# Optimization experiments

Measured on AMD Instinct MI355X. Metric: run time of the kernel, lower is better.

## Reference

```python
import jax, jax.numpy as jnp
import numpy as np

EMBED_DIM = 1024
NUM_HEADS = 16
DIM_K = EMBED_DIM // NUM_HEADS
B, S = 2, 2048


def setup_inputs() -> dict:
    key = jax.random.key(0)
    ks = jax.random.split(key, 7)
    scale = 1.0 / np.sqrt(EMBED_DIM)
    return {
        "query": jax.random.normal(ks[0], (B, S, EMBED_DIM), dtype=jnp.float32),
        "key": jax.random.normal(ks[1], (B, S, EMBED_DIM), dtype=jnp.float32),
        "value": jax.random.normal(ks[2], (B, S, EMBED_DIM), dtype=jnp.float32),
        "Wq": jax.random.normal(ks[3], (EMBED_DIM, EMBED_DIM), dtype=jnp.float32) * scale,
        "Wk": jax.random.normal(ks[4], (EMBED_DIM, EMBED_DIM), dtype=jnp.float32) * scale,
        "Wv": jax.random.normal(ks[5], (EMBED_DIM, EMBED_DIM), dtype=jnp.float32) * scale,
        "Wo": jax.random.normal(ks[6], (EMBED_DIM, EMBED_DIM), dtype=jnp.float32) * scale,
    }


def reference(query, key, value, Wq, Wk, Wv, Wo):
    b, s, e = query.shape
    # nn.Linear: y = x @ W.T  (bias=False)
    def proj(x, W):
        y = x @ W.T  # [b, s, e]
        return y.reshape(b, -1, NUM_HEADS, DIM_K).transpose(0, 2, 1, 3)  # [b, h, s, dk]

    q = proj(query, Wq)
    k = proj(key, Wk)
    v = proj(value, Wv)

    # attention: scores = q k^T / sqrt(dk); softmax; @ v  (dropout p=0 in eval)
    scores = jnp.einsum("bhqd,bhkd->bhqk", q, k) / jnp.sqrt(jnp.float32(DIM_K))
    attn = jax.nn.softmax(scores, axis=-1)
    x = jnp.einsum("bhqk,bhkd->bhqd", attn, v)  # [b, h, s, dk]

    x = x.transpose(0, 2, 1, 3).reshape(b, -1, e)  # merge heads
    return x @ Wo.T
```

## Files before the change

### kernel.cpp

```cpp
#include <hip/hip_runtime.h>
#include <hip/hip_bf16.h>
#include <stdint.h>

#define EMBED 1024
#define NHEAD 16
#define DKD   64
#define BATCH 2
#define SEQ   2048
#define MROWS (BATCH*SEQ)

typedef __attribute__((ext_vector_type(8)))  short bf16x8;
typedef __attribute__((ext_vector_type(4)))  float f32x4;
typedef __attribute__((ext_vector_type(16))) float f32x16;
typedef unsigned short u16;
typedef unsigned int   u32;
typedef __attribute__((ext_vector_type(4))) u32 u32x4;

__device__ inline u16 f2bf(float f) {
  return __builtin_bit_cast(u16, __float2bfloat16(f));
}

__device__ inline u32 cvtpk(float lo, float hi) {
  u32 r;
  asm("v_cvt_pk_bf16_f32 %0, %1, %2" : "=v"(r) : "v"(lo), "v"(hi));
  return r;
}

__device__ inline void plswap(u32& x, u32& y) {
  asm volatile("v_permlane32_swap_b32 %0, %1" : "+v"(x), "+v"(y));
}

__device__ inline void gload_lds16(const u16* g, u16* l) {
  __builtin_amdgcn_global_load_lds(
      (const __attribute__((address_space(1))) u32*)(const void*)g,
      (__attribute__((address_space(3))) u32*)(void*)l, 16, 0, 0);
}

__global__ __launch_bounds__(256) void cast_w(
    const float* __restrict__ s0, const float* __restrict__ s1,
    const float* __restrict__ s2, const float* __restrict__ s3,
    u16* __restrict__ d0, u16* __restrict__ d1, u16* __restrict__ d2,
    u16* __restrict__ d3) {
  const int y = blockIdx.y;
  const float* s = (y == 0) ? s0 : (y == 1) ? s1 : (y == 2) ? s2 : s3;
  u16* d        = (y == 0) ? d0 : (y == 1) ? d1 : (y == 2) ? d2 : d3;
  constexpr int n4 = EMBED * EMBED / 4;
  int i = blockIdx.x * 256 + threadIdx.x;
  int stride = gridDim.x * 256;
  for (int idx = i; idx < n4; idx += stride) {
    float4 f = ((const float4*)s)[idx];
    ushort4 o;
    o.x = f2bf(f.x); o.y = f2bf(f.y); o.z = f2bf(f.z); o.w = f2bf(f.w);
    ((ushort4*)d)[idx] = o;
  }
}

__global__ __launch_bounds__(256)
void gemm_qkv(const float* __restrict__ A0, const float* __restrict__ A1,
              const float* __restrict__ A2, const u16* __restrict__ B0,
              const u16* __restrict__ B1, const u16* __restrict__ B2,
              u16* __restrict__ C0, u16* __restrict__ C1, u16* __restrict__ C2) {
  constexpr int K = EMBED;
  __shared__ u16 As[128 * 32];
  __shared__ u16 Bs[128 * 32];
  const int z = blockIdx.z;
  const float* A = (z == 0) ? A0 : (z == 1) ? A1 : A2;
  const u16* B   = (z == 0) ? B0 : (z == 1) ? B1 : B2;
  u16* C         = (z == 0) ? C0 : (z == 1) ? C1 : C2;

  const int t = threadIdx.x;
  const int w = t >> 6, l = t & 63;
  const int lr = l & 15, lg = l >> 4;
  const int fid = blockIdx.x;
  const int mblk = 4 * (fid & 7) + (fid >> 6);
  const int nblk = (fid >> 3) & 7;
  const int m0 = mblk * 128;
  const int n0 = nblk * 128;
  const int wr = (w >> 1) * 64, wc = (w & 1) * 64;

  f32x4 acc[4][4] = {};

  const int srow = t >> 2;
  const int scol = (t & 3) * 8;
  const float* Agf = A + (size_t)(m0 + srow) * K + scol;
  const u16*   Bg  = B + (size_t)(n0 + srow) * K + scol;
  u16* BsW = Bs + w * 512;
  const size_t rowstep = (size_t)64 * K;

  auto loadA = [&](float4 (&f)[4], int k0) {
    f[0] = *(const float4*)(Agf + k0);
    f[1] = *(const float4*)(Agf + k0 + 4);
    f[2] = *(const float4*)(Agf + k0 + rowstep);
    f[3] = *(const float4*)(Agf + k0 + rowstep + 4);
  };

  float4 fa[4];
  loadA(fa, 0);
  for (int k0 = 0; k0 < K; k0 += 32) {
    u32x4 pa0 = {cvtpk(fa[0].x, fa[0].y), cvtpk(fa[0].z, fa[0].w),
                 cvtpk(fa[1].x, fa[1].y), cvtpk(fa[1].z, fa[1].w)};
    u32x4 pa1 = {cvtpk(fa[2].x, fa[2].y), cvtpk(fa[2].z, fa[2].w),
                 cvtpk(fa[3].x, fa[3].y), cvtpk(fa[3].z, fa[3].w)};
    *(u32x4*)(As + w * 512 + l * 8)        = pa0;
    *(u32x4*)(As + 2048 + w * 512 + l * 8) = pa1;
    gload_lds16(Bg + k0,           BsW);
    gload_lds16(Bg + k0 + rowstep, BsW + 64 * 32);
    if (k0 + 32 < K) loadA(fa, k0 + 32);
    __syncthreads();
    bf16x8 a[4], b[4];
#pragma unroll
    for (int r = 0; r < 4; r++)
      a[r] = *(const bf16x8*)(As + (wr + r * 16 + lr) * 32 + 8 * lg);
#pragma unroll
    for (int c = 0; c < 4; c++)
      b[c] = *(const bf16x8*)(Bs + (wc + c * 16 + lr) * 32 + 8 * lg);
#pragma unroll
    for (int r = 0; r < 4; r++)
#pragma unroll
      for (int c = 0; c < 4; c++)
        acc[r][c] = __builtin_amdgcn_mfma_f32_16x16x32_bf16(a[r], b[c], acc[r][c], 0, 0, 0);
    __syncthreads();
  }

  const float esc = (z == 0) ? 0.18033688f : 1.0f;
#pragma unroll
  for (int r = 0; r < 4; r++)
#pragma unroll
    for (int c = 0; c < 4; c++)
#pragma unroll
      for (int j = 0; j < 4; j++) {
        int m = m0 + wr + r * 16 + lg * 4 + j;
        int n = n0 + wc + c * 16 + lr;
        int b_ = m >> 11, s_ = m & 2047;
        int h_ = n >> 6,  d_ = n & 63;
        u16 vv = f2bf(acc[r][c][j] * esc);
        if (z == 2)
          C[((size_t)(b_ * NHEAD + h_) * DKD + d_) * SEQ + s_] = vv;
        else
          C[(((size_t)(b_ * NHEAD + h_) * SEQ + s_) << 6) + d_] = vv;
      }
}

__global__ __launch_bounds__(256)
void gemm_out(const u16* __restrict__ A, const u16* __restrict__ B,
              float* __restrict__ C) {
  constexpr int K = EMBED, N = EMBED;
  __shared__ u16 As[64 * 32];
  __shared__ u16 Bs[128 * 32];
  const int t = threadIdx.x;
  const int w = t >> 6, l = t & 63;
  const int lr = l & 15, lg = l >> 4;
  const int fid = blockIdx.x;
  const int mblk = 8 * (fid & 7) + (fid >> 6);
  const int nblk = (fid >> 3) & 7;
  const int m0 = mblk * 64;
  const int n0 = nblk * 128;
  const int wr = (w >> 1) * 32, wc = (w & 1) * 64;

  f32x4 acc[2][4] = {};

  const int srow = t >> 2;
  const int scol = (t & 3) * 8;
  const u16* Ag = A + (size_t)(m0 + srow) * K + scol;
  const u16* Bg = B + (size_t)(n0 + srow) * K + scol;
  u16* AsW = As + w * 512;
  u16* BsW = Bs + w * 512;
  const size_t rowstep = (size_t)64 * K;

  for (int k0 = 0; k0 < K; k0 += 32) {
    gload_lds16(Ag + k0,           AsW);
    gload_lds16(Bg + k0,           BsW);
    gload_lds16(Bg + k0 + rowstep, BsW + 64 * 32);
    __syncthreads();
    bf16x8 a[2], b[4];
#pragma unroll
    for (int r = 0; r < 2; r++)
      a[r] = *(const bf16x8*)(As + (wr + r * 16 + lr) * 32 + 8 * lg);
#pragma unroll
    for (int c = 0; c < 4; c++)
      b[c] = *(const bf16x8*)(Bs + (wc + c * 16 + lr) * 32 + 8 * lg);
#pragma unroll
    for (int r = 0; r < 2; r++)
#pragma unroll
      for (int c = 0; c < 4; c++)
        acc[r][c] = __builtin_amdgcn_mfma_f32_16x16x32_bf16(a[r], b[c], acc[r][c], 0, 0, 0);
    __syncthreads();
  }

#pragma unroll
  for (int r = 0; r < 2; r++)
#pragma unroll
    for (int c = 0; c < 4; c++)
#pragma unroll
      for (int j = 0; j < 4; j++) {
        int m = m0 + wr + r * 16 + lg * 4 + j;
        int n = n0 + wc + c * 16 + lr;
        C[(size_t)m * N + n] = acc[r][c][j];
      }
}

__global__ __launch_bounds__(256, 2)
void attn_kernel(const u16* __restrict__ Qh, const u16* __restrict__ Kh,
                 const u16* __restrict__ Vt, u16* __restrict__ Xo) {
  __shared__ u16 KV[4][8192];
  const int t = threadIdx.x, w = t >> 6, l = t & 63;
  const int q32 = l & 31, h = l >> 5;
  const int xcd = blockIdx.x & 7;
  const int li  = blockIdx.x >> 3;
  const int bh  = xcd * 4 + (li >> 4);
  const int qblk = li & 15;
  const int b_ = bh >> 4, h_ = bh & 15;
  const size_t base = (size_t)bh * SEQ * DKD;
  const u16* Kb = Kh + base;
  const u16* Vb = Vt + base;
  constexpr int NT = SEQ / 64;
  constexpr float NM = -1.442695041f;

  const int qrow = qblk * 128 + w * 32 + q32;
  bf16x8 qf[4];
#pragma unroll
  for (int ks = 0; ks < 4; ks++)
    qf[ks] = *(const bf16x8*)(Qh + base + (size_t)qrow * DKD + ks * 16 + h * 8);

  const u32 one2 = 0x3F803F80u;
  const bf16x8 ones = __builtin_bit_cast(bf16x8, (u32x4){one2, one2, one2, one2});
  f32x16 nmv;
#pragma unroll
  for (int r = 0; r < 16; r++) nmv[r] = NM;

  f32x16 acc[2] = {};
  f32x16 lacc = {};

  auto stage = [&](int slot, int kt) {
    u16* kd = &KV[slot][0];
    u16* vd = &KV[slot][4096];
    const int rb = w * 8 + (l >> 3);
    const int sg = (l & 7) ^ (l >> 3);
#pragma unroll
    for (int ch = 0; ch < 2; ch++) {
      int row = ch * 32 + rb;
      gload_lds16(Kb + (size_t)(kt * 64 + row) * DKD + sg * 8,
                  kd + (ch * 32 + w * 8) * 64);
      gload_lds16(Vb + (size_t)row * SEQ + kt * 64 + sg * 8,
                  vd + (ch * 32 + w * 8) * 64);
    }
  };

  auto qk = [&](const u16* kd, f32x16 (&s)[2]) {
#pragma unroll
    for (int c = 0; c < 2; c++) {
      int row = c * 32 + q32;
#pragma unroll
      for (int ks = 0; ks < 4; ks++) {
        bf16x8 kf = *(const bf16x8*)(kd + row * 64 + (((2 * ks + h) ^ (row & 7)) * 8));
        s[c] = __builtin_amdgcn_mfma_f32_32x32x16_bf16(kf, qf[ks], s[c], 0, 0, 0);
      }
    }
  };
  auto vload = [&](const u16* vd, bf16x8 (&vf)[2][4]) {
#pragma unroll
    for (int dc = 0; dc < 2; dc++) {
      int row = dc * 32 + q32;
#pragma unroll
      for (int tile = 0; tile < 4; tile++)
        vf[dc][tile] = *(const bf16x8*)(vd + row * 64 + (((2 * tile + h) ^ (row & 7)) * 8));
    }
  };
  auto exp_pack = [&](f32x16 (&s)[2], bf16x8 (&pfrag)[4]) {
#pragma unroll
    for (int c = 0; c < 2; c++) {
      float p[16];
#pragma unroll
      for (int r = 0; r < 16; r++)
        p[r] = __builtin_amdgcn_exp2f(s[c][r]);
      u32 Pk[8];
#pragma unroll
      for (int i = 0; i < 8; i++) Pk[i] = cvtpk(p[2 * i], p[2 * i + 1]);
      plswap(Pk[0], Pk[2]); plswap(Pk[1], Pk[3]);
      plswap(Pk[4], Pk[6]); plswap(Pk[5], Pk[7]);
      pfrag[2 * c]     = __builtin_bit_cast(bf16x8, (u32x4){Pk[0], Pk[1], Pk[2], Pk[3]});
      pfrag[2 * c + 1] = __builtin_bit_cast(bf16x8, (u32x4){Pk[4], Pk[5], Pk[6], Pk[7]});
    }
  };
  auto pv = [&](bf16x8 (&vf)[2][4], bf16x8 (&pfrag)[4]) {
#pragma unroll
    for (int tile = 0; tile < 4; tile++) {
#pragma unroll
      for (int dc = 0; dc < 2; dc++)
        acc[dc] = __builtin_amdgcn_mfma_f32_32x32x16_bf16(vf[dc][tile], pfrag[tile], acc[dc], 0, 0, 0);
      lacc = __builtin_amdgcn_mfma_f32_32x32x16_bf16(ones, pfrag[tile], lacc, 0, 0, 0);
    }
  };

  stage(0, 0);
  stage(1, 1);
  __syncthreads();

  for (int kt = 0; kt < NT; kt += 2) {
    const int sA = kt & 3, sB = (kt + 1) & 3;
    if (kt + 2 < NT) {
      stage((kt + 2) & 3, kt + 2);
      stage((kt + 3) & 3, kt + 3);
    }
    f32x16 scA[2], scB[2];
    scA[0] = nmv; scA[1] = nmv; scB[0] = nmv; scB[1] = nmv;
    qk(&KV[sA][0], scA);
    qk(&KV[sB][0], scB);
    bf16x8 vfA[2][4];
    vload(&KV[sA][4096], vfA);
    bf16x8 pfA[4];
    exp_pack(scA, pfA);
    pv(vfA, pfA);
    bf16x8 vfB[2][4];
    vload(&KV[sB][4096], vfB);
    bf16x8 pfB[4];
    exp_pack(scB, pfB);
    pv(vfB, pfB);
    __syncthreads();
  }

  float inv = 1.0f / lacc[0];
  u16* orow = Xo + ((size_t)b_ * SEQ + qrow) * EMBED + h_ * DKD;
#pragma unroll
  for (int dc = 0; dc < 2; dc++)
#pragma unroll
    for (int k4 = 0; k4 < 4; k4++) {
      u32 w0 = cvtpk(acc[dc][4 * k4 + 0] * inv, acc[dc][4 * k4 + 1] * inv);
      u32 w1 = cvtpk(acc[dc][4 * k4 + 2] * inv, acc[dc][4 * k4 + 3] * inv);
      int d = dc * 32 + k4 * 8 + h * 4;
      uint2 pk; pk.x = w0; pk.y = w1;
      *(uint2*)(orow + d) = pk;
    }
}

extern "C" void kernel_launch(void* const* d_in, const int* in_sizes, int n_in,
                              void* d_out, int out_size, void* d_ws, size_t ws_size,
                              hipStream_t stream) {
  const float* q  = (const float*)d_in[0];
  const float* k  = (const float*)d_in[1];
  const float* v  = (const float*)d_in[2];
  const float* Wq = (const float*)d_in[3];
  const float* Wk = (const float*)d_in[4];
  const float* Wv = (const float*)d_in[5];
  const float* Wo = (const float*)d_in[6];

  char* ws = (char*)d_ws;
  const size_t SZ_X = (size_t)MROWS * EMBED * 2;
  const size_t SZ_W = (size_t)EMBED * EMBED * 2;
  u16* wqb  = (u16*)(ws + 3 * SZ_X);
  u16* wkb  = (u16*)(ws + 3 * SZ_X + SZ_W);
  u16* wvb  = (u16*)(ws + 3 * SZ_X + 2 * SZ_W);
  u16* wob  = (u16*)(ws + 3 * SZ_X + 3 * SZ_W);
  u16* Qh   = (u16*)(ws + 3 * SZ_X + 4 * SZ_W);
  u16* Kh   = (u16*)(ws + 4 * SZ_X + 4 * SZ_W);
  u16* Vt   = (u16*)(ws + 5 * SZ_X + 4 * SZ_W);
  u16* Xcat = (u16*)(ws + 6 * SZ_X + 4 * SZ_W);

  cast_w<<<dim3(128, 4), 256, 0, stream>>>(Wq, Wk, Wv, Wo, wqb, wkb, wvb, wob);

  gemm_qkv<<<dim3(256, 1, 3), 256, 0, stream>>>(
      q, k, v, wqb, wkb, wvb, Qh, Kh, Vt);

  attn_kernel<<<512, 256, 0, stream>>>(Qh, Kh, Vt, Xcat);

  gemm_out<<<512, 256, 0, stream>>>(Xcat, wob, (float*)d_out);
}
```

Before: 110.6 us.

## Stage fp32 A tiles directly to LDS via async loads, convert on read

The QKV projection GEMM now copies fp32 activation tiles straight into shared memory with global_load_lds, using an XOR-swizzled layout. Conversion to bf16 happens after the LDS read instead of before the LDS write. This drops the register prefetch and conversion stage. In exchange it doubles the LDS footprint for A, converts each value redundantly across waves, and loses the overlap the previous register prefetch gave between the next tile's global load and the current tile's compute.

```diff
diff --git a/kernel.cpp b/kernel.cpp
--- a/kernel.cpp
+++ b/kernel.cpp
@@ -31,6 +31,11 @@
 }
 
 __device__ inline void gload_lds16(const u16* g, u16* l) {
+  __builtin_amdgcn_global_load_lds(
+      (const __attribute__((address_space(1))) u32*)(const void*)g,
+      (__attribute__((address_space(3))) u32*)(void*)l, 16, 0, 0);
+}
+__device__ inline void gload_lds16f(const float* g, float* l) {
   __builtin_amdgcn_global_load_lds(
       (const __attribute__((address_space(1))) u32*)(const void*)g,
       (__attribute__((address_space(3))) u32*)(void*)l, 16, 0, 0);
@@ -61,8 +66,8 @@
               const u16* __restrict__ B1, const u16* __restrict__ B2,
               u16* __restrict__ C0, u16* __restrict__ C1, u16* __restrict__ C2) {
   constexpr int K = EMBED;
-  __shared__ u16 As[128 * 32];
-  __shared__ u16 Bs[128 * 32];
+  __shared__ float Asf[128 * 32];
+  __shared__ u16   Bs[128 * 32];
   const int z = blockIdx.z;
   const float* A = (z == 0) ? A0 : (z == 1) ? A1 : A2;
   const u16* B   = (z == 0) ? B0 : (z == 1) ? B1 : B2;
@@ -82,35 +87,36 @@
 
   const int srow = t >> 2;
   const int scol = (t & 3) * 8;
-  const float* Agf = A + (size_t)(m0 + srow) * K + scol;
-  const u16*   Bg  = B + (size_t)(n0 + srow) * K + scol;
+  const u16* Bg = B + (size_t)(n0 + srow) * K + scol;
   u16* BsW = Bs + w * 512;
   const size_t rowstep = (size_t)64 * K;
 
-  auto loadA = [&](float4 (&f)[4], int k0) {
-    f[0] = *(const float4*)(Agf + k0);
-    f[1] = *(const float4*)(Agf + k0 + 4);
-    f[2] = *(const float4*)(Agf + k0 + rowstep);
-    f[3] = *(const float4*)(Agf + k0 + rowstep + 4);
-  };
-
-  float4 fa[4];
-  loadA(fa, 0);
+  const int sg = (l & 7) ^ (l >> 3);
+  const float* Agf = A + (size_t)m0 * K + sg * 4;
+  auto stageA = [&](int k0) {
+#pragma unroll
+    for (int i = 0; i < 4; i++) {
+      int row = i * 32 + w * 8 + (l >> 3);
+      gload_lds16f(Agf + (size_t)row * K + k0, Asf + (i * 32 + w * 8) * 32);
+    }
+  };
+
   for (int k0 = 0; k0 < K; k0 += 32) {
-    u32x4 pa0 = {cvtpk(fa[0].x, fa[0].y), cvtpk(fa[0].z, fa[0].w),
-                 cvtpk(fa[1].x, fa[1].y), cvtpk(fa[1].z, fa[1].w)};
-    u32x4 pa1 = {cvtpk(fa[2].x, fa[2].y), cvtpk(fa[2].z, fa[2].w),
-                 cvtpk(fa[3].x, fa[3].y), cvtpk(fa[3].z, fa[3].w)};
-    *(u32x4*)(As + w * 512 + l * 8)        = pa0;
-    *(u32x4*)(As + 2048 + w * 512 + l * 8) = pa1;
+    stageA(k0);
     gload_lds16(Bg + k0,           BsW);
     gload_lds16(Bg + k0 + rowstep, BsW + 64 * 32);
-    if (k0 + 32 < K) loadA(fa, k0 + 32);
     __syncthreads();
     bf16x8 a[4], b[4];
 #pragma unroll
-    for (int r = 0; r < 4; r++)
-      a[r] = *(const bf16x8*)(As + (wr + r * 16 + lr) * 32 + 8 * lg);
+    for (int r = 0; r < 4; r++) {
+      int row = wr + r * 16 + lr;
+      int key = lr & 7;
+      f32x4 lo = *(const f32x4*)(Asf + row * 32 + (((2 * lg)     ^ key) * 4));
+      f32x4 hi = *(const f32x4*)(Asf + row * 32 + (((2 * lg + 1) ^ key) * 4));
+      a[r] = __builtin_bit_cast(bf16x8,
+              (u32x4){cvtpk(lo[0], lo[1]), cvtpk(lo[2], lo[3]),
+                      cvtpk(hi[0], hi[1]), cvtpk(hi[2], hi[3])});
+    }
 #pragma unroll
     for (int c = 0; c < 4; c++)
       b[c] = *(const bf16x8*)(Bs + (wc + c * 16 + lr) * 32 + 8 * lg);
```

Result: slower. 114.0 us (+3.1%).
